# Performance work log

Measured on AMD Instinct MI355X. Metric: run time of the kernel, lower is better.

## Reference

```python
import jax, jax.numpy as jnp
import numpy as np

B, S, D, H = 2, 2048, 512, 8
DK = D // H

def setup_inputs() -> dict:
    key = jax.random.key(0)
    ks = jax.random.split(key, 13)
    inp = {
        'query': jax.random.normal(ks[0], (B, S, D), jnp.float32),
        'key': jax.random.normal(ks[1], (B, S, D), jnp.float32),
        'value': jax.random.normal(ks[2], (B, S, D), jnp.float32),
        'group_prob': jax.random.uniform(ks[3], (B, S, S), jnp.float32),
        'mask': jax.random.randint(ks[4], (B, S, S), 0, 2, jnp.int32),
        'Wq': jax.random.normal(ks[5], (D, D), jnp.float32) * 0.02,
        'bq': jax.random.normal(ks[6], (D,), jnp.float32) * 0.02,
        'Wk': jax.random.normal(ks[7], (D, D), jnp.float32) * 0.02,
        'bk': jax.random.normal(ks[8], (D,), jnp.float32) * 0.02,
        'Wv': jax.random.normal(ks[9], (D, D), jnp.float32) * 0.02,
        'bv': jax.random.normal(ks[10], (D,), jnp.float32) * 0.02,
        'Wo': jax.random.normal(ks[11], (D, D), jnp.float32) * 0.02,
        'bo': jax.random.normal(ks[12], (D,), jnp.float32) * 0.02,
    }
    return inp

def reference(query, key, value, group_prob, mask, Wq, bq, Wk, bk, Wv, bv, Wo, bo):
    # project and split heads: [B,S,D] -> [B,H,S,dk]
    def proj(x, W, b):
        return (x @ W.T + b).reshape(B, S, H, DK).transpose(0, 2, 1, 3)
    q = proj(query, Wq, bq)
    k = proj(key, Wk, bk)
    v = proj(value, Wv, bv)
    scale = 1.0 / np.sqrt(DK).astype(np.float32)
    scores = jnp.einsum('bhqd,bhkd->bhqk', q, k) * scale  # [B,H,S,S]
    # allowed = mask | identity-diagonal; disallowed positions get -1e9
    diag = jnp.eye(S, dtype=bool)
    allowed = (mask.astype(bool) | diag)[:, None, :, :]  # [B,1,S,S]
    scores = jnp.where(allowed, scores, jnp.float32(-1e9))
    p_attn = jax.nn.softmax(scores, axis=-1) * group_prob[:, None, :, :]
    # dropout is identity in eval/deterministic mode
    x = jnp.einsum('bhqk,bhkd->bhqd', p_attn, v)  # [B,H,S,dk]
    x = x.transpose(0, 2, 1, 3).reshape(B, S, D)
    return x @ Wo.T + bo
```

## Files before the change

kernel.cpp:

```cpp
#include <hip/hip_runtime.h>
#include <hip/hip_bf16.h>
#include <cstdint>
#include <cstddef>

typedef __attribute__((ext_vector_type(8))) short bf16x8;
typedef __attribute__((ext_vector_type(4))) float f32x4;
typedef __attribute__((address_space(3))) void lds_void;
typedef const __attribute__((address_space(1))) void g_void;

constexpr int Bc = 2, Sc = 2048, Dc = 512, Hc = 8, DKc = 64;
constexpr int SPLIT = 2;
constexpr int NKT = Sc / 64;
constexpr int KT_PER = NKT / SPLIT;
constexpr float CSC = 0.18033688011112042f;

struct alignas(16) us8 { unsigned short u[8]; };
struct alignas(8) us4 { unsigned short u[4]; };

__device__ __forceinline__ unsigned short f2bf(float x) {
  union { float f; unsigned int u; } v; v.f = x;
  unsigned int r = (v.u + 0x7FFFu + ((v.u >> 16) & 1u)) >> 16;
  return (unsigned short)r;
}

__device__ __forceinline__ float bf2f(unsigned short u) {
  union { unsigned int u; float f; } v; v.u = ((unsigned int)u) << 16;
  return v.f;
}

__device__ __forceinline__ us8 cvt8(float4 a, float4 b) {
  us8 o;
  o.u[0] = f2bf(a.x); o.u[1] = f2bf(a.y); o.u[2] = f2bf(a.z); o.u[3] = f2bf(a.w);
  o.u[4] = f2bf(b.x); o.u[5] = f2bf(b.y); o.u[6] = f2bf(b.z); o.u[7] = f2bf(b.w);
  return o;
}

struct PArgs {
  const float* g; const int* m; unsigned short* gp;
  const float* wsrc[4]; unsigned short* wdst[4];
};

__global__ __launch_bounds__(256)
void prepass(PArgs pa)
{
  const int bx = blockIdx.x;
  const int tid = threadIdx.x;
  if (bx < 2048) {
    const int idx = bx;
    const int b = idx >> 10, rest = idx & 1023, qt = rest >> 5, kt = rest & 31;
    const int colb = tid & 15, hi = (tid >> 4) & 3, wid = tid >> 6;
    const int q = qt * 64 + wid * 16 + colb;
    const int k0 = kt * 64 + hi * 4;
    const float* grow = pa.g + ((size_t)b * Sc + q) * Sc + k0;
    const int* mrow = pa.m + ((size_t)b * Sc + q) * Sc + k0;
    unsigned short vals[16];
#pragma unroll
    for (int n = 0; n < 4; ++n) {
      float4 gv = *(const float4*)(grow + n * 16);
      int4 mv = *(const int4*)(mrow + n * 16);
      const int kb = k0 + n * 16;
      const float gg[4] = {gv.x, gv.y, gv.z, gv.w};
      const int mm[4] = {mv.x, mv.y, mv.z, mv.w};
#pragma unroll
      for (int rr = 0; rr < 4; ++rr) {
        const bool allowed = (mm[rr] != 0) || (kb + rr == q);
        vals[n * 4 + rr] = allowed ? (unsigned short)(f2bf(gg[rr]) | 1u) : (unsigned short)0;
      }
    }
    us8* o = (us8*)(pa.gp + (((size_t)idx * 256) + tid) * 16);
    o[0] = *(us8*)&vals[0];
    o[1] = *(us8*)&vals[8];
  } else {
    const int r = bx - 2048;
    const int wi = r >> 3, sub = r & 7;
    const float* s = pa.wsrc[wi];
    unsigned short* d = pa.wdst[wi];
#pragma unroll
    for (int t = 0; t < 16; ++t) {
      const int i = sub * 4096 + t * 256 + tid;
      float4 a = ((const float4*)s)[(size_t)i * 2];
      float4 b = ((const float4*)s)[(size_t)i * 2 + 1];
      ((us8*)d)[i] = cvt8(a, b);
    }
  }
}

struct GArgs {
  const void* A[3];
  const unsigned short* W[3];
  const float* bias[3];
  void* C[3];
  int mode[3];
  float osc[3];
};

template<int A_FP32>
__global__ __launch_bounds__(256)
void gemm_bn64(GArgs ga)
{
  __shared__ unsigned short As[128][64];
  __shared__ unsigned short Bs[64][64];

  constexpr int K = 512, N = 512;
  const int z = blockIdx.z;
  const unsigned short* Wp = ga.W[z];
  const float* bias = ga.bias[z];
  const int mode = ga.mode[z];
  const float osc = ga.osc[z];

  const int tid = threadIdx.x, lane = tid & 63, w = tid >> 6;
  const int m0 = blockIdx.x * 128, n0 = blockIdx.y * 64;
  const int wm = w >> 1, wn = w & 1;
  const int colb = lane & 15, hi = lane >> 4, rowb = hi * 4;
  const int swz = (colb & 7) << 4;

  f32x4 acc[4][2];
#pragma unroll
  for (int i = 0; i < 4; ++i)
#pragma unroll
    for (int j = 0; j < 2; ++j) acc[i][j] = (f32x4){0.f, 0.f, 0.f, 0.f};

  const int lrow8 = lane >> 3;
  const int cb = ((lane & 7) * 16) ^ (lrow8 << 4);

  for (int k0 = 0; k0 < K; k0 += 64) {
    if (k0) __syncthreads();
#pragma unroll
    for (int i = 0; i < 2; ++i) {
      const int u = w + i * 4;
      const int row = u * 8 + lrow8;
      const unsigned short* bsrc = Wp + (size_t)(n0 + row) * K + k0 + (cb >> 1);
      __builtin_amdgcn_global_load_lds((g_void*)bsrc, (lds_void*)((char*)&Bs[0][0] + u * 1024), 16, 0, 0);
    }
    if (A_FP32) {
      const float* Af = (const float*)ga.A[z];
#pragma unroll
      for (int i = 0; i < 4; ++i) {
        const int u = w * 4 + i;
        const int row = u * 8 + lrow8;
        const float* src = Af + (size_t)(m0 + row) * K + k0 + (cb >> 1);
        float4 v0 = *(const float4*)src, v1 = *(const float4*)(src + 4);
        *(us8*)((char*)&As[0][0] + u * 1024 + lane * 16) = cvt8(v0, v1);
      }
    } else {
      const unsigned short* Ab = (const unsigned short*)ga.A[z];
#pragma unroll
      for (int i = 0; i < 4; ++i) {
        const int u = w * 4 + i;
        const int row = u * 8 + lrow8;
        const unsigned short* asrc = Ab + (size_t)(m0 + row) * K + k0 + (cb >> 1);
        __builtin_amdgcn_global_load_lds((g_void*)asrc, (lds_void*)((char*)&As[0][0] + u * 1024), 16, 0, 0);
      }
    }
    asm volatile("s_waitcnt vmcnt(0)" ::: "memory");
    __syncthreads();

    char* ab = (char*)&As[0][0];
    char* bb = (char*)&Bs[0][0];
#pragma unroll
    for (int kk = 0; kk < 2; ++kk) {
      bf16x8 af[4], bfr[2];
#pragma unroll
      for (int mf = 0; mf < 4; ++mf) {
        const int ar = wm * 64 + mf * 16 + colb;
        af[mf] = *(const bf16x8*)(ab + ar * 128 + ((kk * 64 + hi * 16) ^ swz));
      }
#pragma unroll
      for (int nf = 0; nf < 2; ++nf) {
        const int br = wn * 32 + nf * 16 + colb;
        bfr[nf] = *(const bf16x8*)(bb + br * 128 + ((kk * 64 + hi * 16) ^ swz));
      }
      __builtin_amdgcn_s_setprio(1);
#pragma unroll
      for (int mf = 0; mf < 4; ++mf)
#pragma unroll
        for (int nf = 0; nf < 2; ++nf)
          acc[mf][nf] = __builtin_amdgcn_mfma_f32_16x16x32_bf16(af[mf], bfr[nf], acc[mf][nf], 0, 0, 0);
      __builtin_amdgcn_s_setprio(0);
    }
  }

#pragma unroll
  for (int nf = 0; nf < 2; ++nf) {
    const int gn = n0 + wn * 32 + nf * 16 + colb;
    const float bv = bias[gn];
    if (mode == 1) {
      unsigned short* Cp = (unsigned short*)ga.C[z];
#pragma unroll
      for (int mf = 0; mf < 4; ++mf) {
        const int gm = m0 + wm * 64 + mf * 16 + rowb;
        const int bb_ = gm >> 11, ss = gm & (Sc - 1);
        us4 vv;
#pragma unroll
        for (int rr = 0; rr < 4; ++rr) vv.u[rr] = f2bf(acc[mf][nf][rr] + bv);
        *(us4*)(Cp + ((size_t)bb_ * N + gn) * Sc + ss) = vv;
      }
    } else if (mode == 0) {
      unsigned short* Cp = (unsigned short*)ga.C[z];
#pragma unroll
      for (int mf = 0; mf < 4; ++mf)
#pragma unroll
        for (int rr = 0; rr < 4; ++rr) {
          const int gm = m0 + wm * 64 + mf * 16 + rowb + rr;
          Cp[(size_t)gm * N + gn] = f2bf((acc[mf][nf][rr] + bv) * osc);
        }
    } else {
      float* Cp = (float*)ga.C[z];
#pragma unroll
      for (int mf = 0; mf < 4; ++mf)
#pragma unroll
        for (int rr = 0; rr < 4; ++rr) {
          const int gm = m0 + wm * 64 + mf * 16 + rowb + rr;
          Cp[(size_t)gm * N + gn] = acc[mf][nf][rr] + bv;
        }
    }
  }
}

__global__ __launch_bounds__(256, 4)
void attn_split(const unsigned short* __restrict__ Qb,
                const unsigned short* __restrict__ Kb,
                const unsigned short* __restrict__ Vt,
                const unsigned short* __restrict__ Gp,
                unsigned short* __restrict__ Pacc,
                float* __restrict__ Pml)
{
  __shared__ unsigned short Ks[2][64][64];
  __shared__ unsigned short Vs[2][64][64];
  __shared__ unsigned short Ps[4][16][64];

  const int tid = threadIdx.x, lane = tid & 63, wid = tid >> 6;
  const int bh = blockIdx.x, b = bh >> 3, h = bh & 7;
  const int qt = blockIdx.y, q0 = qt * 64;
  const int sp = blockIdx.z;
  const int kt0 = sp * KT_PER;

  const int colb = lane & 15;
  const int hi = lane >> 4;
  const int rowb = hi * 4;
  const int c3s = (colb & 7) << 4;

  bf16x8 qf[2];
  {
    const unsigned short* qp = Qb + ((size_t)(b * Sc + q0 + wid * 16 + colb) * Dc + h * DKc + hi * 8);
    qf[0] = *(const bf16x8*)qp;
    qf[1] = *(const bf16x8*)(qp + 32);
  }

  f32x4 acc[4] = {{0,0,0,0},{0,0,0,0},{0,0,0,0},{0,0,0,0}};
  float lrun = 0.f;

  auto stageKV = [&](int bufI, int kt) {
    const int k0 = kt * 64;
#pragma unroll
    for (int i = 0; i < 2; ++i) {
      const int obase = wid * 1024 + i * 4096;
      const int row = (obase >> 7) + (lane >> 3);
      const int cb = ((lane & 7) * 16) ^ ((row & 7) << 4);
      const unsigned short* ksrc = Kb + (size_t)(b * Sc + k0 + row) * Dc + h * DKc + (cb >> 1);
      const unsigned short* vsrc = Vt + ((size_t)b * Dc + h * DKc + row) * Sc + k0 + (cb >> 1);
      __builtin_amdgcn_global_load_lds((g_void*)ksrc, (lds_void*)((char*)&Ks[bufI][0][0] + obase), 16, 0, 0);
      __builtin_amdgcn_global_load_lds((g_void*)vsrc, (lds_void*)((char*)&Vs[bufI][0][0] + obase), 16, 0, 0);
    }
  };

  const unsigned short* gtile = Gp + (((size_t)(b * 1024 + qt * 32)) * 256 + tid) * 16;
  us8 gcur0, gcur1;
  auto loadG = [&](int kt, us8& g0, us8& g1) {
    const us8* p = (const us8*)(gtile + (size_t)kt * 4096);
    g0 = p[0]; g1 = p[1];
  };

  stageKV(0, kt0);
  loadG(kt0, gcur0, gcur1);
  asm volatile("s_waitcnt vmcnt(0)" ::: "memory");
  __syncthreads();

  int buf = 0;
  char* psbase = (char*)&Ps[wid][0][0];

  for (int j = 0; j < KT_PER; ++j) {
    const int kt = kt0 + j;
    us8 gn0, gn1;
    if (j + 1 < KT_PER) {
      stageKV(buf ^ 1, kt + 1);
      loadG(kt + 1, gn0, gn1);
    }

    f32x4 sf[4] = {{0,0,0,0},{0,0,0,0},{0,0,0,0},{0,0,0,0}};
    char* ksb = (char*)&Ks[buf][0][0];
    __builtin_amdgcn_s_setprio(1);
#pragma unroll
    for (int kk = 0; kk < 2; ++kk) {
#pragma unroll
      for (int n = 0; n < 4; ++n) {
        const int krow = n * 16 + colb;
        bf16x8 kf = *(const bf16x8*)(ksb + krow * 128 + ((kk * 64 + hi * 16) ^ ((krow & 7) << 4)));
        sf[n] = __builtin_amdgcn_mfma_f32_16x16x32_bf16(kf, qf[kk], sf[n], 0, 0, 0);
      }
    }
    __builtin_amdgcn_s_setprio(0);

    unsigned int pw[8];
#pragma unroll
    for (int n = 0; n < 4; ++n) {
#pragma unroll
      for (int s2 = 0; s2 < 2; ++s2) {
        const int jv = n * 4 + s2 * 2;
        const unsigned short u0 = (jv < 8) ? gcur0.u[jv] : gcur1.u[jv - 8];
        const unsigned short u1 = (jv + 1 < 8) ? gcur0.u[jv + 1] : gcur1.u[jv + 1 - 8];
        const float p0 = __builtin_amdgcn_exp2f(sf[n][s2 * 2]);
        const float p1 = __builtin_amdgcn_exp2f(sf[n][s2 * 2 + 1]);
        lrun = fmaf(p0, (float)(u0 & 1u), lrun);
        lrun = fmaf(p1, (float)(u1 & 1u), lrun);
        const float q0v = p0 * bf2f(u0), q1v = p1 * bf2f(u1);
        asm("v_cvt_pk_bf16_f32 %0, %1, %2" : "=v"(pw[n * 2 + s2]) : "v"(q0v), "v"(q1v));
      }
    }

#pragma unroll
    for (int n = 0; n < 4; ++n) {
      const unsigned long long w64 = ((unsigned long long)pw[n * 2 + 1] << 32) | pw[n * 2];
      *(unsigned long long*)(psbase + colb * 128 + ((n * 32 + hi * 8) ^ c3s)) = w64;
    }

    char* vsb = (char*)&Vs[buf][0][0];
    __builtin_amdgcn_s_setprio(1);
#pragma unroll
    for (int kk = 0; kk < 2; ++kk) {
      bf16x8 pf = *(const bf16x8*)(psbase + colb * 128 + ((kk * 64 + hi * 16) ^ c3s));
#pragma unroll
      for (int n = 0; n < 4; ++n) {
        const int vrow = n * 16 + colb;
        bf16x8 vf = *(const bf16x8*)(vsb + vrow * 128 + ((kk * 64 + hi * 16) ^ ((vrow & 7) << 4)));
        acc[n] = __builtin_amdgcn_mfma_f32_16x16x32_bf16(vf, pf, acc[n], 0, 0, 0);
      }
    }
    __builtin_amdgcn_s_setprio(0);

    asm volatile("s_waitcnt vmcnt(0)" ::: "memory");
    __syncthreads();
    buf ^= 1;
    if (j + 1 < KT_PER) { gcur0 = gn0; gcur1 = gn1; }
  }

  lrun += __shfl_xor(lrun, 16);
  lrun += __shfl_xor(lrun, 32);

  const size_t blin = ((size_t)bh * 32 + qt) * SPLIT + sp;
  unsigned short* pa = Pacc + blin * 4096;
#pragma unroll
  for (int n = 0; n < 4; ++n)
#pragma unroll
    for (int rr = 0; rr < 4; ++rr)
      pa[(size_t)(n * 16 + rowb + rr) * 64 + wid * 16 + colb] = f2bf(acc[n][rr]);
  if (hi == 0) Pml[blin * 64 + wid * 16 + colb] = lrun;
}

__global__ __launch_bounds__(256)
void attn_reduce(const unsigned short* __restrict__ Pacc, const float* __restrict__ Pml,
                 unsigned short* __restrict__ Xb)
{
  const int gidx = blockIdx.x;
  const int bh = gidx >> 5, qt = gidx & 31;
  const int b = bh >> 3, h = bh & 7;
  const int tid = threadIdx.x;
  const int qi = tid & 63;
  const int d0 = (tid >> 6) * 16;
  const size_t pb = (size_t)gidx * SPLIT;

  float denom = 0.f;
#pragma unroll
  for (int s = 0; s < SPLIT; ++s) denom += Pml[(pb + s) * 64 + qi];
  const float inv = 1.0f / denom;

  unsigned short vals[16];
#pragma unroll
  for (int j = 0; j < 16; ++j) {
    float a = 0.f;
#pragma unroll
    for (int s = 0; s < SPLIT; ++s)
      a += bf2f(Pacc[(pb + s) * 4096 + (size_t)(d0 + j) * 64 + qi]);
    vals[j] = f2bf(a * inv);
  }
  unsigned short* xp = Xb + ((size_t)(b * Sc) + qt * 64 + qi) * Dc + h * DKc + d0;
  *(us8*)xp = *(us8*)&vals[0];
  *(us8*)(xp + 8) = *(us8*)&vals[8];
}

extern "C" void kernel_launch(void* const* d_in, const int* in_sizes, int n_in,
                              void* d_out, int out_size, void* d_ws, size_t ws_size,
                              hipStream_t stream)
{
  const float* query = (const float*)d_in[0];
  const float* key_  = (const float*)d_in[1];
  const float* value = (const float*)d_in[2];
  const float* gprob = (const float*)d_in[3];
  const int*   mask  = (const int*)d_in[4];
  const float* Wq = (const float*)d_in[5];
  const float* bq = (const float*)d_in[6];
  const float* Wk = (const float*)d_in[7];
  const float* bk = (const float*)d_in[8];
  const float* Wv = (const float*)d_in[9];
  const float* bv = (const float*)d_in[10];
  const float* Wo = (const float*)d_in[11];
  const float* bo = (const float*)d_in[12];
  float* out = (float*)d_out;

  const size_t elems = (size_t)Bc * Sc * Dc;
  const size_t gelems = (size_t)Bc * Sc * Sc;
  const size_t welems = (size_t)Dc * Dc;

  char* base = (char*)d_ws;
  unsigned short* Qb = (unsigned short*)(base);
  unsigned short* Kb = Qb + elems;
  unsigned short* Vt = Kb + elems;
  unsigned short* Xb = Vt + elems;
  unsigned short* Gp = Xb + elems;
  unsigned short* Wqb = Gp + gelems;
  unsigned short* Wkb = Wqb + welems;
  unsigned short* Wvb = Wkb + welems;
  unsigned short* Wob = Wvb + welems;
  unsigned short* Pacc = Wob + welems;
  float* Pml = (float*)(Pacc + (size_t)(Bc * Hc) * 32 * SPLIT * 4096);

  PArgs pa;
  pa.g = gprob; pa.m = mask; pa.gp = Gp;
  pa.wsrc[0] = Wq; pa.wdst[0] = Wqb;
  pa.wsrc[1] = Wk; pa.wdst[1] = Wkb;
  pa.wsrc[2] = Wv; pa.wdst[2] = Wvb;
  pa.wsrc[3] = Wo; pa.wdst[3] = Wob;
  hipLaunchKernelGGL(prepass, dim3(2080), dim3(256), 0, stream, pa);

  GArgs gq;
  gq.A[0] = (const void*)query; gq.W[0] = Wqb; gq.bias[0] = bq; gq.C[0] = (void*)Qb; gq.mode[0] = 0; gq.osc[0] = CSC;
  gq.A[1] = (const void*)key_;  gq.W[1] = Wkb; gq.bias[1] = bk; gq.C[1] = (void*)Kb; gq.mode[1] = 0; gq.osc[1] = 1.0f;
  gq.A[2] = (const void*)value; gq.W[2] = Wvb; gq.bias[2] = bv; gq.C[2] = (void*)Vt; gq.mode[2] = 1; gq.osc[2] = 1.0f;
  hipLaunchKernelGGL((gemm_bn64<1>), dim3(32, 8, 3), dim3(256), 0, stream, gq);

  dim3 ga(Bc * Hc, Sc / 64, SPLIT);
  hipLaunchKernelGGL(attn_split, ga, dim3(256), 0, stream, Qb, Kb, Vt, Gp, Pacc, Pml);
  hipLaunchKernelGGL(attn_reduce, dim3(Bc * Hc * 32), dim3(256), 0, stream, Pacc, Pml, Xb);

  GArgs go;
  go.A[0] = (const void*)Xb; go.W[0] = Wob; go.bias[0] = bo; go.C[0] = (void*)out; go.mode[0] = 2; go.osc[0] = 1.0f;
  go.A[1] = go.A[0]; go.W[1] = go.W[0]; go.bias[1] = go.bias[0]; go.C[1] = go.C[0]; go.mode[1] = 2; go.osc[1] = 1.0f;
  go.A[2] = go.A[0]; go.W[2] = go.W[0]; go.bias[2] = go.bias[0]; go.C[2] = go.C[0]; go.mode[2] = 2; go.osc[2] = 1.0f;
  hipLaunchKernelGGL((gemm_bn64<0>), dim3(32, 8, 1), dim3(256), 0, stream, go);
}
```

Baseline: 96.62 us.

## Remap attention grid for XCD-local group_prob reuse and unroll tile loop by two

Switches the attention kernel to a 1D grid and decodes the block index so that all 16 (head, split) blocks sharing one (batch, query-tile) land on the same XCD. They then reuse the same group_prob and Q rows from that XCD's L2. The tile loop is also manually unrolled by two with ping-pong register sets for the prefetched group_prob, removing the runtime buffer index and the register copies. The row-sum accumulator is split into four independent chains to shorten the dependency chain. The cost is more live registers and reliance on the round-robin XCD dispatch assumption.

```diff
diff --git a/kernel.cpp b/kernel.cpp
--- a/kernel.cpp
+++ b/kernel.cpp
@@ -230,9 +230,14 @@
   __shared__ unsigned short Ps[4][16][64];
 
   const int tid = threadIdx.x, lane = tid & 63, wid = tid >> 6;
-  const int bh = blockIdx.x, b = bh >> 3, h = bh & 7;
-  const int qt = blockIdx.y, q0 = qt * 64;
-  const int sp = blockIdx.z;
+  const int wgid = blockIdx.x;
+  const int xcd = wgid & 7, rest = wgid >> 3;
+  const int mem = rest & 15, ghi = rest >> 4;
+  const int g = ghi * 8 + xcd;
+  const int b = g >> 5, qt = g & 31;
+  const int h = mem >> 1, sp = mem & 1;
+  const int bh = b * 8 + h;
+  const int q0 = qt * 64;
   const int kt0 = sp * KT_PER;
 
   const int colb = lane & 15;
@@ -248,7 +253,7 @@
   }
 
   f32x4 acc[4] = {{0,0,0,0},{0,0,0,0},{0,0,0,0},{0,0,0,0}};
-  float lrun = 0.f;
+  float lr0 = 0.f, lr1 = 0.f, lr2 = 0.f, lr3 = 0.f;
 
   auto stageKV = [&](int bufI, int kt) {
     const int k0 = kt * 64;
@@ -265,30 +270,27 @@
   };
 
   const unsigned short* gtile = Gp + (((size_t)(b * 1024 + qt * 32)) * 256 + tid) * 16;
-  us8 gcur0, gcur1;
   auto loadG = [&](int kt, us8& g0, us8& g1) {
     const us8* p = (const us8*)(gtile + (size_t)kt * 4096);
     g0 = p[0]; g1 = p[1];
   };
 
+  us8 gA0, gA1, gB0, gB1;
   stageKV(0, kt0);
-  loadG(kt0, gcur0, gcur1);
+  loadG(kt0, gA0, gA1);
   asm volatile("s_waitcnt vmcnt(0)" ::: "memory");
   __syncthreads();
 
-  int buf = 0;
   char* psbase = (char*)&Ps[wid][0][0];
 
-  for (int j = 0; j < KT_PER; ++j) {
-    const int kt = kt0 + j;
-    us8 gn0, gn1;
-    if (j + 1 < KT_PER) {
-      stageKV(buf ^ 1, kt + 1);
+  auto doTile = [&](int kt, int bufI, us8& gc0, us8& gc1, us8& gn0, us8& gn1) {
+    if (kt + 1 < kt0 + KT_PER) {
+      stageKV(bufI ^ 1, kt + 1);
       loadG(kt + 1, gn0, gn1);
     }
 
     f32x4 sf[4] = {{0,0,0,0},{0,0,0,0},{0,0,0,0},{0,0,0,0}};
-    char* ksb = (char*)&Ks[buf][0][0];
+    char* ksb = (char*)&Ks[bufI][0][0];
     __builtin_amdgcn_s_setprio(1);
 #pragma unroll
     for (int kk = 0; kk < 2; ++kk) {
@@ -304,18 +306,21 @@
     unsigned int pw[8];
 #pragma unroll
     for (int n = 0; n < 4; ++n) {
+      float lacc = 0.f;
 #pragma unroll
       for (int s2 = 0; s2 < 2; ++s2) {
         const int jv = n * 4 + s2 * 2;
-        const unsigned short u0 = (jv < 8) ? gcur0.u[jv] : gcur1.u[jv - 8];
-        const unsigned short u1 = (jv + 1 < 8) ? gcur0.u[jv + 1] : gcur1.u[jv + 1 - 8];
+        const unsigned short u0 = (jv < 8) ? gc0.u[jv] : gc1.u[jv - 8];
+        const unsigned short u1 = (jv + 1 < 8) ? gc0.u[jv + 1] : gc1.u[jv + 1 - 8];
         const float p0 = __builtin_amdgcn_exp2f(sf[n][s2 * 2]);
         const float p1 = __builtin_amdgcn_exp2f(sf[n][s2 * 2 + 1]);
-        lrun = fmaf(p0, (float)(u0 & 1u), lrun);
-        lrun = fmaf(p1, (float)(u1 & 1u), lrun);
+        lacc = fmaf(p0, (float)(u0 & 1u), lacc);
+        lacc = fmaf(p1, (float)(u1 & 1u), lacc);
         const float q0v = p0 * bf2f(u0), q1v = p1 * bf2f(u1);
         asm("v_cvt_pk_bf16_f32 %0, %1, %2" : "=v"(pw[n * 2 + s2]) : "v"(q0v), "v"(q1v));
       }
+      if (n == 0) lr0 += lacc; else if (n == 1) lr1 += lacc;
+      else if (n == 2) lr2 += lacc; else lr3 += lacc;
     }
 
 #pragma unroll
@@ -324,7 +329,7 @@
       *(unsigned long long*)(psbase + colb * 128 + ((n * 32 + hi * 8) ^ c3s)) = w64;
     }
 
-    char* vsb = (char*)&Vs[buf][0][0];
+    char* vsb = (char*)&Vs[bufI][0][0];
     __builtin_amdgcn_s_setprio(1);
 #pragma unroll
     for (int kk = 0; kk < 2; ++kk) {
@@ -340,10 +345,14 @@
 
     asm volatile("s_waitcnt vmcnt(0)" ::: "memory");
     __syncthreads();
-    buf ^= 1;
-    if (j + 1 < KT_PER) { gcur0 = gn0; gcur1 = gn1; }
-  }
-
+  };
+
+  for (int j = 0; j < KT_PER; j += 2) {
+    doTile(kt0 + j,     0, gA0, gA1, gB0, gB1);
+    doTile(kt0 + j + 1, 1, gB0, gB1, gA0, gA1);
+  }
+
+  float lrun = (lr0 + lr1) + (lr2 + lr3);
   lrun += __shfl_xor(lrun, 16);
   lrun += __shfl_xor(lrun, 32);
 
@@ -438,8 +447,7 @@
   gq.A[2] = (const void*)value; gq.W[2] = Wvb; gq.bias[2] = bv; gq.C[2] = (void*)Vt; gq.mode[2] = 1; gq.osc[2] = 1.0f;
   hipLaunchKernelGGL((gemm_bn64<1>), dim3(32, 8, 3), dim3(256), 0, stream, gq);
 
-  dim3 ga(Bc * Hc, Sc / 64, SPLIT);
-  hipLaunchKernelGGL(attn_split, ga, dim3(256), 0, stream, Qb, Kb, Vt, Gp, Pacc, Pml);
+  hipLaunchKernelGGL(attn_split, dim3(1024), dim3(256), 0, stream, Qb, Kb, Vt, Gp, Pacc, Pml);
   hipLaunchKernelGGL(attn_reduce, dim3(Bc * Hc * 32), dim3(256), 0, stream, Pacc, Pml, Xb);
 
   GArgs go;
```

New measurement: 93.42 us. 1.03x faster.
